# Kernel tuning notes

Hardware: AMD Instinct MI355X
Metric: run time of the kernel (lower is better)

Reference implementation:

```python
import jax, jax.numpy as jnp
import numpy as np

B, L, W = 64, 20, 48
D = W * W           # 2304, MoE input/output size (image_width**2)
E = 4               # num_experts
HID = 2 * D         # expert hidden size
K = 1               # top_k
LOSS_COEF = 1e-2


def _cv_squared(x):
    # torch: x.var() (unbiased) / (x.mean()**2 + eps)
    eps = 1e-10
    return jnp.var(x, ddof=1) / (jnp.mean(x) ** 2 + eps)


def _moe(x, w_gate, w1, b1, w2, b2):
    # Noisy top-k gating, inference path (train=False => clean logits, no noise).
    logits = x @ w_gate                                   # [B, E]
    top_logits, top_idx = jax.lax.top_k(logits, K + 1)    # min(k+1, E)
    topk_gates = jax.nn.softmax(top_logits[:, :K], axis=-1)
    gates = jnp.zeros_like(logits).at[
        jnp.arange(x.shape[0])[:, None], top_idx[:, :K]
    ].set(topk_gates)                                     # [B, E] sparse gates
    importance = gates.sum(0)
    load = (gates > 0).sum(0).astype(x.dtype)             # _gates_to_load
    aux = LOSS_COEF * (_cv_squared(importance) + _cv_squared(load))
    # Dense expert compute weighted by gates (same math as dispatch/combine).
    h = jax.nn.relu(jnp.einsum('bd,edh->beh', x, w1) + b1)      # [B,E,HID]
    y = jnp.einsum('beh,ehd->bed', h, w2) + b2                  # [B,E,D]
    out = jnp.einsum('be,bed->bd', gates, y)                    # [B,D]
    return out, aux


def _conv3d(x, w, b, pad):
    y = jax.lax.conv_general_dilated(
        x, w, window_strides=(1, 1, 1), padding=pad,
        dimension_numbers=('NCDHW', 'OIDHW', 'NCDHW'))
    return y + b[None, :, None, None, None]


def _forward(input, conv1_w, conv1_b, conv2_w, conv2_b,
             t_gate, t_w1, t_b1, t_w2, t_b2,
             a_gate, a_w1, a_b1, a_w2, a_b2,
             q_gate, q_w1, q_b1, q_w2, q_b2,
             enc_w, enc_b, dec_w, dec_b):
    x = jnp.transpose(input, (0, 2, 1, 3, 4))                   # [B,1,L,H,W]
    x = jax.nn.relu(_conv3d(x, conv1_w, conv1_b, ((1, 1), (1, 1), (1, 1))))
    x = jax.nn.relu(_conv3d(x, conv2_w, conv2_b, ((0, 0), (1, 1), (1, 1))))  # [B,1,1,H,W]
    xf = x.reshape(x.shape[0], -1)                              # [B, D]
    transform, l1 = _moe(xf, t_gate, t_w1, t_b1, t_w2, t_b2)
    add, l2 = _moe(xf, a_gate, a_w1, a_b1, a_w2, a_b2)
    quad, l3 = _moe(xf, q_gate, q_w1, q_b1, q_w2, q_b2)
    s = input.shape                                             # [B,L,1,H,W]
    transform = transform.reshape(s[0], 1, s[2], s[3], s[4])
    add = add.reshape(s[0], 1, s[2], s[3], s[4])
    quad = quad.reshape(s[0], 1, s[2], s[3], s[4])
    out = input * input * quad + input * transform + add        # [B,L,1,H,W]
    # encoder = Linear(D,D)+ReLU, decoder = Linear(D,D) over flattened H*W
    of = out.reshape(s[0], s[1], D)
    of = jax.nn.relu(of @ enc_w + enc_b)
    of = of @ dec_w + dec_b
    of = jax.nn.sigmoid(of)
    return of.reshape(s), l1 + l2 + l3


def setup_inputs() -> dict:
    key = jax.random.key(0)
    ks = jax.random.split(key, 32)
    sc = 0.02
    inp = {
        'input': jax.random.normal(ks[0], (B, L, 1, W, W), jnp.float32),
        'conv1_w': jax.random.normal(ks[1], (10, 1, 3, 3, 3), jnp.float32) * sc,
        'conv1_b': jnp.zeros((10,), jnp.float32),
        'conv2_w': jax.random.normal(ks[2], (1, 10, L, 3, 3), jnp.float32) * sc,
        'conv2_b': jnp.zeros((1,), jnp.float32),
        'enc_w': jax.random.normal(ks[3], (D, D), jnp.float32) * sc,
        'enc_b': jnp.zeros((D,), jnp.float32),
        'dec_w': jax.random.normal(ks[4], (D, D), jnp.float32) * sc,
        'dec_b': jnp.zeros((D,), jnp.float32),
    }
    for i, p in enumerate(['t', 'a', 'q']):
        k0, k1, k2 = jax.random.split(ks[5 + i], 3)
        inp[p + '_gate'] = jnp.zeros((D, E), jnp.float32) + jax.random.normal(k0, (D, E), jnp.float32) * sc
        inp[p + '_w1'] = jax.random.normal(k1, (E, D, HID), jnp.float32) * sc
        inp[p + '_b1'] = jnp.zeros((E, HID), jnp.float32)
        inp[p + '_w2'] = jax.random.normal(k2, (E, HID, D), jnp.float32) * sc
        inp[p + '_b2'] = jnp.zeros((E, D), jnp.float32)
    return inp


def reference(input, conv1_w, conv1_b, conv2_w, conv2_b,
              t_gate, t_w1, t_b1, t_w2, t_b2,
              a_gate, a_w1, a_b1, a_w2, a_b2,
              q_gate, q_w1, q_b1, q_w2, q_b2,
              enc_w, enc_b, dec_w, dec_b):
    return _forward(input, conv1_w, conv1_b, conv2_w, conv2_b,
                    t_gate, t_w1, t_b1, t_w2, t_b2,
                    a_gate, a_w1, a_b1, a_w2, a_b2,
                    q_gate, q_w1, q_b1, q_w2, q_b2,
                    enc_w, enc_b, dec_w, dec_b)
```

## Files before the change

kernel.cpp:

```cpp
#include <hip/hip_runtime.h>
#include <stdint.h>

#define NB 64
#define NL 20
#define ND 2304
#define NE 4
#define NH 4608
#define NM 1280

typedef float f32x4 __attribute__((ext_vector_type(4)));
typedef __bf16 bf16x8 __attribute__((ext_vector_type(8)));
typedef unsigned short u16;
typedef u16 u16x4 __attribute__((ext_vector_type(4)));
typedef unsigned int u32;
typedef u32 u32x4 __attribute__((ext_vector_type(4)));

__device__ __forceinline__ u16 f2bf(float f) {
  u32 u = __builtin_bit_cast(u32, f);
  u += 0x7fffu + ((u >> 16) & 1u);
  return (u16)(u >> 16);
}

#define OFF_XFACC 0
#define OFF_XF    147456
#define OFF_H     294912
#define OFF_Y     1179648
#define OFF_AUX   1622016
#define OFF_CNT   1622020
#define OFF_ROWS  1622032
#define OFF_OFB   1622240
#define OFF_H1B   3096800
#define OFF_ENCWB 4571360
#define OFF_DECWB 7225568
#define OFF_XC    9879776
#define OFF_P     10322144

__global__ __launch_bounds__(256) void k_zero(float* __restrict__ p) {
  p[(size_t)blockIdx.x * 256 + threadIdx.x] = 0.f;
}

__global__ __launch_bounds__(256) void k_conv(
    const float* __restrict__ in, const float* __restrict__ w1,
    const float* __restrict__ b1, const float* __restrict__ w2,
    float* __restrict__ xf_acc) {
  __shared__ float insl[3][50][50];
  __shared__ float c1[2][50][50];
  __shared__ float w1s[270];
  __shared__ float w2s[90];
  __shared__ float b1s[10];
  const int d = blockIdx.x, b = blockIdx.y, t = threadIdx.x;
  for (int i = t; i < 270; i += 256) w1s[i] = w1[i];
  for (int i = t; i < 90; i += 256) w2s[i] = w2[(size_t)((i / 9) * 20 + d) * 9 + (i % 9)];
  if (t < 10) b1s[t] = b1[t];
  for (int i = t; i < 7500; i += 256) {
    int s = i / 2500, rr = (i % 2500) / 50, cc = i % 50;
    int gd = d - 1 + s, gy = rr - 1, gx = cc - 1;
    float v = 0.f;
    if (gd >= 0 && gd < NL && (unsigned)gy < 48u && (unsigned)gx < 48u)
      v = in[((size_t)b * NL + gd) * ND + gy * 48 + gx];
    insl[s][rr][cc] = v;
  }
  for (int i = t; i < 5000; i += 256) ((float*)c1)[i] = 0.f;
  float s2[3][4];
#pragma unroll
  for (int qi = 0; qi < 3; ++qi)
#pragma unroll
    for (int xq = 0; xq < 4; ++xq) s2[qi][xq] = 0.f;
  __syncthreads();
  for (int pc = 0; pc < 5; ++pc) {
#pragma unroll
    for (int qi = 0; qi < 3; ++qi) {
      int q = t + qi * 256;
      if (q < 576) {
        int y = q / 12, x0 = (q % 12) * 4;
        float a0[4], a1[4];
        const float bb0 = b1s[2 * pc], bb1 = b1s[2 * pc + 1];
#pragma unroll
        for (int xq = 0; xq < 4; ++xq) { a0[xq] = bb0; a1[xq] = bb1; }
#pragma unroll
        for (int kd = 0; kd < 3; ++kd)
#pragma unroll
          for (int ky = 0; ky < 3; ++ky) {
            float v[6];
#pragma unroll
            for (int i = 0; i < 6; ++i) v[i] = insl[kd][y + ky][x0 + i];
            const float* wa = &w1s[(2 * pc) * 27 + kd * 9 + ky * 3];
            const float* wb = wa + 27;
#pragma unroll
            for (int xq = 0; xq < 4; ++xq) {
              a0[xq] += v[xq] * wa[0] + v[xq + 1] * wa[1] + v[xq + 2] * wa[2];
              a1[xq] += v[xq] * wb[0] + v[xq + 1] * wb[1] + v[xq + 2] * wb[2];
            }
          }
#pragma unroll
        for (int xq = 0; xq < 4; ++xq) {
          c1[0][y + 1][x0 + 1 + xq] = fmaxf(a0[xq], 0.f);
          c1[1][y + 1][x0 + 1 + xq] = fmaxf(a1[xq], 0.f);
        }
      }
    }
    __syncthreads();
#pragma unroll
    for (int qi = 0; qi < 3; ++qi) {
      int q = t + qi * 256;
      if (q < 576) {
        int y = q / 12, x0 = (q % 12) * 4;
#pragma unroll
        for (int cc = 0; cc < 2; ++cc) {
#pragma unroll
          for (int ky = 0; ky < 3; ++ky) {
            float v[6];
#pragma unroll
            for (int i = 0; i < 6; ++i) v[i] = c1[cc][y + ky][x0 + i];
            const float* wr = &w2s[(2 * pc + cc) * 9 + ky * 3];
#pragma unroll
            for (int xq = 0; xq < 4; ++xq)
              s2[qi][xq] += v[xq] * wr[0] + v[xq + 1] * wr[1] + v[xq + 2] * wr[2];
          }
        }
      }
    }
    __syncthreads();
  }
#pragma unroll
  for (int qi = 0; qi < 3; ++qi) {
    int q = t + qi * 256;
    if (q < 576) {
#pragma unroll
      for (int xq = 0; xq < 4; ++xq)
        atomicAdd(&xf_acc[(size_t)b * ND + q * 4 + xq], s2[qi][xq]);
    }
  }
}

__global__ __launch_bounds__(256) void k_bias_relu(
    const float* __restrict__ acc, const float* __restrict__ c2b, float* __restrict__ xf) {
  size_t i = (size_t)blockIdx.x * 256 + threadIdx.x;
  xf[i] = fmaxf(acc[i] + c2b[0], 0.f);
}

__global__ __launch_bounds__(256) void k_gate(
    const float* __restrict__ xf,
    const float* __restrict__ g0, const float* __restrict__ g1, const float* __restrict__ g2,
    float* __restrict__ aux, int* __restrict__ cnt, int* __restrict__ rows) {
  const int p = blockIdx.x, t = threadIdx.x;
  const float* __restrict__ g = (p == 0) ? g0 : ((p == 1) ? g1 : g2);
  __shared__ float lg[64][4];
  __shared__ int lidx[64];
  __shared__ int lcnt[4];
  if (t < 4) lcnt[t] = 0;
  const int wv = t >> 6, l = t & 63;
  for (int b0 = 0; b0 < 64; b0 += 4) {
    int bb = b0 + wv;
    f32x4 acc = {0.f, 0.f, 0.f, 0.f};
    const float* xr = xf + (size_t)bb * ND + l * 36;
    const float* gr = g + (size_t)l * 36 * 4;
#pragma unroll
    for (int i4 = 0; i4 < 9; ++i4) {
      f32x4 xv = *(const f32x4*)(xr + i4 * 4);
#pragma unroll
      for (int qq = 0; qq < 4; ++qq) {
        f32x4 gv = *(const f32x4*)(gr + (i4 * 4 + qq) * 4);
        acc += xv[qq] * gv;
      }
    }
#pragma unroll
    for (int e = 0; e < 4; ++e) {
      float pv = acc[e];
#pragma unroll
      for (int off = 32; off > 0; off >>= 1) pv += __shfl_down(pv, off);
      if (l == 0) lg[bb][e] = pv;
    }
  }
  __syncthreads();
  if (t < 64) {
    float best = lg[t][0];
    int bi = 0;
#pragma unroll
    for (int e = 1; e < 4; ++e)
      if (lg[t][e] > best) { best = lg[t][e]; bi = e; }
    lidx[t] = bi;
    atomicAdd(&lcnt[bi], 1);
  }
  __syncthreads();
  if (t == 0) {
    int ofs[4]; int run = 0;
#pragma unroll
    for (int e = 0; e < 4; ++e) { ofs[e] = run; run += lcnt[e]; cnt[p * 4 + e] = lcnt[e]; }
    for (int b = 0; b < 64; ++b) { int e = lidx[b]; rows[p * 64 + ofs[e]++] = b; }
    float var = 0.f;
#pragma unroll
    for (int e = 0; e < 4; ++e) { float dd = (float)lcnt[e] - 16.f; var += dd * dd; }
    var *= (1.f / 3.f);
    aux[p] = 0.02f * var / (256.f + 1e-10f);
  }
}

__global__ __launch_bounds__(256) void k_gather(
    const float* __restrict__ xf, const int* __restrict__ rows, float* __restrict__ Xc) {
  const int slot = blockIdx.x, t = threadIdx.x;
  const int p = slot >> 6;
  const int r = rows[slot];
  const f32x4* src = (const f32x4*)(xf + ((size_t)(p * 0 + r)) * ND);
  f32x4* dst = (f32x4*)(Xc + (size_t)slot * ND);
  for (int i = t; i < ND / 4; i += 256) dst[i] = src[i];
}

template <int K, int N, int KS>
__global__ __launch_bounds__(256) void k_moe_stream(
    const float* __restrict__ Xc,
    const float* __restrict__ wt, const float* __restrict__ wa, const float* __restrict__ wq,
    const int* __restrict__ cnt, float* __restrict__ P) {
  constexpr int KL = K / KS;
  constexpr int KW = KL / 4;
  const int tile = blockIdx.x;
  const int ks = blockIdx.y;
  const int pe = blockIdx.z >> 1, ch = blockIdx.z & 1;
  const int p = pe >> 2, e = pe & 3;
  const int c = cnt[p * 4 + e];
  const int rstart = ch * 32;
  if (rstart >= c) return;
  const int nrows = min(32, c - rstart);
  int pref = 0;
  for (int e2 = 0; e2 < e; ++e2) pref += cnt[p * 4 + e2];
  const int slot0 = p * 64 + pref + rstart;
  const float* __restrict__ W = (p == 0) ? wt : ((p == 1) ? wa : wq);
  __shared__ float xs[32][KL + 4];
  const int t = threadIdx.x;
  for (int i = t; i < 32 * (KL / 4); i += 256) {
    int r = i / (KL / 4), kq = (i - r * (KL / 4)) * 4;
    int slot = slot0 + r; if (slot > 191) slot = 191;
    *(f32x4*)(&xs[r][kq]) = *(const f32x4*)(Xc + (size_t)slot * K + ks * KL + kq);
  }
  __syncthreads();
  const int w = t >> 6, l = t & 63;
  const int j0 = tile * 128 + l * 2;
  const float* __restrict__ wp = W + (size_t)e * K * N + (size_t)(ks * KL + w * KW) * N + j0;
  const int kloc = w * KW;
  float acc0[32], acc1[32];
#pragma unroll
  for (int r = 0; r < 32; ++r) { acc0[r] = 0.f; acc1[r] = 0.f; }
  for (int kb = 0; kb < KW; kb += 4) {
    float2 wv0 = *(const float2*)(wp + (size_t)(kb + 0) * N);
    float2 wv1 = *(const float2*)(wp + (size_t)(kb + 1) * N);
    float2 wv2 = *(const float2*)(wp + (size_t)(kb + 2) * N);
    float2 wv3 = *(const float2*)(wp + (size_t)(kb + 3) * N);
#pragma unroll
    for (int rg = 0; rg < 8; ++rg) {
      if (rg * 4 < nrows) {
#pragma unroll
        for (int rr = 0; rr < 4; ++rr) {
          const int r = rg * 4 + rr;
          f32x4 xv = *(const f32x4*)(&xs[r][kloc + kb]);
          acc0[r] = fmaf(xv[0], wv0.x, acc0[r]);
          acc1[r] = fmaf(xv[0], wv0.y, acc1[r]);
          acc0[r] = fmaf(xv[1], wv1.x, acc0[r]);
          acc1[r] = fmaf(xv[1], wv1.y, acc1[r]);
          acc0[r] = fmaf(xv[2], wv2.x, acc0[r]);
          acc1[r] = fmaf(xv[2], wv2.y, acc1[r]);
          acc0[r] = fmaf(xv[3], wv3.x, acc0[r]);
          acc1[r] = fmaf(xv[3], wv3.y, acc1[r]);
        }
      }
    }
  }
  float* red = &xs[0][0];
  const size_t pbase = (size_t)ks * 192 * N;
#pragma unroll
  for (int b = 0; b < 4; ++b) {
    __syncthreads();
#pragma unroll
    for (int rr = 0; rr < 8; ++rr) {
      const int r = b * 8 + rr;
      *(float2*)(&red[((w * 8 + rr) * 64 + l) * 2]) = make_float2(acc0[r], acc1[r]);
    }
    __syncthreads();
#pragma unroll
    for (int s = 0; s < 2; ++s) {
      const int rr = w * 2 + s;
      const int r = b * 8 + rr;
      if (r < nrows) {
        float2 s0 = *(const float2*)(&red[((0 * 8 + rr) * 64 + l) * 2]);
        float2 s1 = *(const float2*)(&red[((1 * 8 + rr) * 64 + l) * 2]);
        float2 s2 = *(const float2*)(&red[((2 * 8 + rr) * 64 + l) * 2]);
        float2 s3 = *(const float2*)(&red[((3 * 8 + rr) * 64 + l) * 2]);
        float2 o = make_float2(s0.x + s1.x + s2.x + s3.x, s0.y + s1.y + s2.y + s3.y);
        *(float2*)(P + pbase + (size_t)(slot0 + r) * N + j0) = o;
      }
    }
  }
}

__global__ __launch_bounds__(256) void k_red1(
    const float* __restrict__ P,
    const float* __restrict__ b1t, const float* __restrict__ b1a, const float* __restrict__ b1q,
    const int* __restrict__ cnt, float* __restrict__ H) {
  const int slot = blockIdx.y;
  const int p = slot >> 6, pos = slot & 63;
  int e = 0, run = cnt[p * 4];
  while (pos >= run && e < 3) { ++e; run += cnt[p * 4 + e]; }
  const float* __restrict__ b1 = (p == 0) ? b1t : ((p == 1) ? b1a : b1q);
  const int j0 = blockIdx.x * 1024 + threadIdx.x * 4;
  if (j0 >= NH) return;
  f32x4 s = *(const f32x4*)(b1 + (size_t)e * NH + j0);
#pragma unroll
  for (int ks = 0; ks < 8; ++ks)
    s += *(const f32x4*)(P + ((size_t)ks * 192 + slot) * NH + j0);
  f32x4 r;
#pragma unroll
  for (int q = 0; q < 4; ++q) r[q] = fmaxf(s[q], 0.f);
  *(f32x4*)(H + (size_t)slot * NH + j0) = r;
}

__global__ __launch_bounds__(256) void k_red2(
    const float* __restrict__ P,
    const float* __restrict__ b2t, const float* __restrict__ b2a, const float* __restrict__ b2q,
    const int* __restrict__ cnt, const int* __restrict__ rows, float* __restrict__ Y) {
  const int slot = blockIdx.y;
  const int p = slot >> 6, pos = slot & 63;
  int e = 0, run = cnt[p * 4];
  while (pos >= run && e < 3) { ++e; run += cnt[p * 4 + e]; }
  const float* __restrict__ b2 = (p == 0) ? b2t : ((p == 1) ? b2a : b2q);
  const int b = rows[slot];
  const int t = threadIdx.x;
  if (t >= 192) return;
  const int j0 = blockIdx.x * 768 + t * 4;
  f32x4 s = *(const f32x4*)(b2 + (size_t)e * ND + j0);
#pragma unroll
  for (int ks = 0; ks < 16; ++ks)
    s += *(const f32x4*)(P + ((size_t)ks * 192 + slot) * ND + j0);
  *(f32x4*)(Y + (size_t)(p * 64 + b) * ND + j0) = s;
}

__global__ __launch_bounds__(256) void k_combine(
    const float* __restrict__ in, const float* __restrict__ Y, u16* __restrict__ ofb) {
  const size_t i = (size_t)blockIdx.x * 256 + threadIdx.x;
  const size_t e0 = i * 4;
  const int row = (int)(e0 / ND);
  const int d = (int)(e0 - (size_t)row * ND);
  const int b = row / NL;
  f32x4 v = *(const f32x4*)(in + e0);
  const size_t yb = (size_t)b * ND + d;
  f32x4 tt = *(const f32x4*)(Y + yb);
  f32x4 aa = *(const f32x4*)(Y + (size_t)64 * ND + yb);
  f32x4 qq = *(const f32x4*)(Y + (size_t)128 * ND + yb);
  u16x4 o;
#pragma unroll
  for (int q = 0; q < 4; ++q) {
    float f = v[q] * v[q] * qq[q] + v[q] * tt[q] + aa[q];
    o[q] = f2bf(f);
  }
  *(u16x4*)(ofb + e0) = o;
}

__global__ __launch_bounds__(256) void k_wt(
    const float* __restrict__ encw, const float* __restrict__ decw,
    u16* __restrict__ encb, u16* __restrict__ decb) {
  __shared__ float tl[32][33];
  const float* __restrict__ src = blockIdx.z ? decw : encw;
  u16* __restrict__ dst = blockIdx.z ? decb : encb;
  const int k0 = blockIdx.x * 32, n0 = blockIdx.y * 32;
  const int tx = threadIdx.x & 31, ty = threadIdx.x >> 5;
  for (int r = ty; r < 32; r += 8) tl[r][tx] = src[(size_t)(k0 + r) * ND + n0 + tx];
  __syncthreads();
  for (int r = ty; r < 32; r += 8) dst[(size_t)(n0 + r) * ND + k0 + tx] = f2bf(tl[tx][r]);
}

template <int MODE>
__global__ __launch_bounds__(256) void k_gemm(
    const u16* __restrict__ A, const u16* __restrict__ Bt,
    const float* __restrict__ bias, void* __restrict__ outp,
    const float* __restrict__ aux) {
  __shared__ u16 As[128 * 32];
  __shared__ u16 Bs[128 * 32];
  const int t = threadIdx.x;
  const int bm = blockIdx.x, bn = blockIdx.y;
  const int lane = t & 63;
  const int wr = (t >> 7) & 1, wc = (t >> 6) & 1;
  const int l15 = lane & 15, l4 = lane >> 4;
  f32x4 acc[4][4] = {};
  const int r0 = t >> 2, kc0 = (t & 3) * 8;
  const int r1 = (t + 256) >> 2, kc1 = ((t + 256) & 3) * 8;
  const size_t baseA = (size_t)(bm * 128) * ND;
  const size_t baseB = (size_t)(bn * 128) * ND;
  for (int k0 = 0; k0 < ND; k0 += 32) {
    *(u32x4*)(As + t * 8) = *(const u32x4*)(A + baseA + (size_t)r0 * ND + k0 + kc0);
    *(u32x4*)(Bs + t * 8) = *(const u32x4*)(Bt + baseB + (size_t)r0 * ND + k0 + kc0);
    *(u32x4*)(As + (t + 256) * 8) = *(const u32x4*)(A + baseA + (size_t)r1 * ND + k0 + kc1);
    *(u32x4*)(Bs + (t + 256) * 8) = *(const u32x4*)(Bt + baseB + (size_t)r1 * ND + k0 + kc1);
    __syncthreads();
    bf16x8 af[4], bfr[4];
#pragma unroll
    for (int i = 0; i < 4; ++i) {
      af[i] = *(const bf16x8*)(As + (wr * 64 + i * 16 + l15) * 32 + l4 * 8);
      bfr[i] = *(const bf16x8*)(Bs + (wc * 64 + i * 16 + l15) * 32 + l4 * 8);
    }
#pragma unroll
    for (int mi = 0; mi < 4; ++mi)
#pragma unroll
      for (int ni = 0; ni < 4; ++ni)
        acc[mi][ni] = __builtin_amdgcn_mfma_f32_16x16x32_bf16(af[mi], bfr[ni], acc[mi][ni], 0, 0, 0);
    __syncthreads();
  }
  const int colbase = bn * 128 + wc * 64;
  const int rowbase = bm * 128 + wr * 64;
#pragma unroll
  for (int mi = 0; mi < 4; ++mi) {
#pragma unroll
    for (int ni = 0; ni < 4; ++ni) {
      const int colg = colbase + ni * 16 + l15;
      const float bv = bias[colg];
#pragma unroll
      for (int r = 0; r < 4; ++r) {
        const int rowg = rowbase + mi * 16 + l4 * 4 + r;
        float v = acc[mi][ni][r] + bv;
        if (MODE == 0) {
          ((u16*)outp)[(size_t)rowg * ND + colg] = f2bf(fmaxf(v, 0.f));
        } else {
          ((float*)outp)[(size_t)rowg * ND + colg] = 1.f / (1.f + __expf(-v));
        }
      }
    }
  }
  if (MODE == 1 && bm == 0 && bn == 0 && t == 0)
    ((float*)outp)[(size_t)NM * ND] = aux[0] + aux[1] + aux[2];
}

extern "C" void kernel_launch(void* const* d_in, const int* in_sizes, int n_in,
                              void* d_out, int out_size, void* d_ws, size_t ws_size,
                              hipStream_t stream) {
  (void)in_sizes; (void)n_in; (void)out_size; (void)ws_size;
  const float* input   = (const float*)d_in[0];
  const float* conv1_w = (const float*)d_in[1];
  const float* conv1_b = (const float*)d_in[2];
  const float* conv2_w = (const float*)d_in[3];
  const float* conv2_b = (const float*)d_in[4];
  const float* enc_w   = (const float*)d_in[5];
  const float* enc_b   = (const float*)d_in[6];
  const float* dec_w   = (const float*)d_in[7];
  const float* dec_b   = (const float*)d_in[8];
  const float* gate_t = (const float*)d_in[9];
  const float* w1_t   = (const float*)d_in[10];
  const float* b1_t   = (const float*)d_in[11];
  const float* w2_t   = (const float*)d_in[12];
  const float* b2_t   = (const float*)d_in[13];
  const float* gate_a = (const float*)d_in[14];
  const float* w1_a   = (const float*)d_in[15];
  const float* b1_a   = (const float*)d_in[16];
  const float* w2_a   = (const float*)d_in[17];
  const float* b2_a   = (const float*)d_in[18];
  const float* gate_q = (const float*)d_in[19];
  const float* w1_q   = (const float*)d_in[20];
  const float* b1_q   = (const float*)d_in[21];
  const float* w2_q   = (const float*)d_in[22];
  const float* b2_q   = (const float*)d_in[23];

  float* ws = (float*)d_ws;
  float* xf_acc = ws + OFF_XFACC;
  float* xf     = ws + OFF_XF;
  float* H      = ws + OFF_H;
  float* Y      = ws + OFF_Y;
  float* aux    = ws + OFF_AUX;
  int*   cnt    = (int*)(ws + OFF_CNT);
  int*   rows   = (int*)(ws + OFF_ROWS);
  u16*   ofb    = (u16*)(ws + OFF_OFB);
  u16*   h1b    = (u16*)(ws + OFF_H1B);
  u16*   encwb  = (u16*)(ws + OFF_ENCWB);
  u16*   decwb  = (u16*)(ws + OFF_DECWB);
  float* Xc     = ws + OFF_XC;
  float* P      = ws + OFF_P;

  k_zero<<<576, 256, 0, stream>>>(xf_acc);
  k_conv<<<dim3(20, 64), 256, 0, stream>>>(input, conv1_w, conv1_b, conv2_w, xf_acc);
  k_bias_relu<<<576, 256, 0, stream>>>(xf_acc, conv2_b, xf);
  k_wt<<<dim3(72, 72, 2), 256, 0, stream>>>(enc_w, dec_w, encwb, decwb);
  k_gate<<<3, 256, 0, stream>>>(xf, gate_t, gate_a, gate_q, aux, cnt, rows);
  k_gather<<<192, 256, 0, stream>>>(xf, rows, Xc);
  k_moe_stream<ND, NH, 8><<<dim3(36, 8, 24), 256, 0, stream>>>(Xc, w1_t, w1_a, w1_q, cnt, P);
  k_red1<<<dim3(5, 192), 256, 0, stream>>>(P, b1_t, b1_a, b1_q, cnt, H);
  k_moe_stream<NH, ND, 16><<<dim3(18, 16, 24), 256, 0, stream>>>(H, w2_t, w2_a, w2_q, cnt, P);
  k_red2<<<dim3(3, 192), 256, 0, stream>>>(P, b2_t, b2_a, b2_q, cnt, rows, Y);
  k_combine<<<2880, 256, 0, stream>>>(input, Y, ofb);
  k_gemm<0><<<dim3(10, 18), 256, 0, stream>>>(ofb, encwb, enc_b, (void*)h1b, aux);
  k_gemm<1><<<dim3(10, 18), 256, 0, stream>>>(h1b, decwb, dec_b, d_out, aux);
}
```

Baseline: 573.6 us.

## Double-buffer MoE expert GEMM tiles via direct global-to-LDS loads

Restructures the streaming MoE GEMM kernel so that X and weight tiles of 32 k-values are loaded into double-buffered shared memory with global_load_lds, and the next tile's load overlaps compute on the current one. Each wave now owns 8 rows across the full k-range instead of all 32 rows over a quarter of k, which removes the cross-wave shared-memory reduction and its many barriers. The intent is to hide weight-streaming latency and cut register pressure from 64 accumulators down to 16. The trade-off is a barrier per k-tile, and the early skip of empty row groups is gone, so padded rows are computed anyway.

```diff
diff --git a/kernel.cpp b/kernel.cpp
--- a/kernel.cpp
+++ b/kernel.cpp
@@ -19,6 +19,12 @@
   u32 u = __builtin_bit_cast(u32, f);
   u += 0x7fffu + ((u >> 16) & 1u);
   return (u16)(u >> 16);
+}
+
+__device__ __forceinline__ void gl_lds16(const void* g, void* l) {
+  __builtin_amdgcn_global_load_lds(
+      (const __attribute__((address_space(1))) void*)g,
+      (__attribute__((address_space(3))) void*)l, 16, 0, 0);
 }
 
 #define OFF_XFACC 0
@@ -199,9 +205,8 @@
 __global__ __launch_bounds__(256) void k_gather(
     const float* __restrict__ xf, const int* __restrict__ rows, float* __restrict__ Xc) {
   const int slot = blockIdx.x, t = threadIdx.x;
-  const int p = slot >> 6;
   const int r = rows[slot];
-  const f32x4* src = (const f32x4*)(xf + ((size_t)(p * 0 + r)) * ND);
+  const f32x4* src = (const f32x4*)(xf + (size_t)r * ND);
   f32x4* dst = (f32x4*)(Xc + (size_t)slot * ND);
   for (int i = t; i < ND / 4; i += 256) dst[i] = src[i];
 }
@@ -212,7 +217,7 @@
     const float* __restrict__ wt, const float* __restrict__ wa, const float* __restrict__ wq,
     const int* __restrict__ cnt, float* __restrict__ P) {
   constexpr int KL = K / KS;
-  constexpr int KW = KL / 4;
+  constexpr int NT = KL / 32;
   const int tile = blockIdx.x;
   const int ks = blockIdx.y;
   const int pe = blockIdx.z >> 1, ch = blockIdx.z & 1;
@@ -225,69 +230,69 @@
   for (int e2 = 0; e2 < e; ++e2) pref += cnt[p * 4 + e2];
   const int slot0 = p * 64 + pref + rstart;
   const float* __restrict__ W = (p == 0) ? wt : ((p == 1) ? wa : wq);
-  __shared__ float xs[32][KL + 4];
+  __shared__ float xsb[2][32 * 32];
+  __shared__ float wtb[2][32 * 128];
   const int t = threadIdx.x;
-  for (int i = t; i < 32 * (KL / 4); i += 256) {
-    int r = i / (KL / 4), kq = (i - r * (KL / 4)) * 4;
-    int slot = slot0 + r; if (slot > 191) slot = 191;
-    *(f32x4*)(&xs[r][kq]) = *(const f32x4*)(Xc + (size_t)slot * K + ks * KL + kq);
-  }
+  const int w = t >> 6, l = t & 63;
+  int slotc = slot0 + (t >> 3); if (slotc > 191) slotc = 191;
+  const float* Xg = Xc + (size_t)slotc * K + ks * KL + (t & 7) * 4;
+  const float* Wg = W + (size_t)e * K * N + (size_t)(ks * KL + (t >> 5)) * N
+                      + tile * 128 + (t & 31) * 4;
+
+#define STAGE(BUF, KT)                                                        \
+  {                                                                           \
+    const int k0_ = (KT) * 32;                                                \
+    gl_lds16(Xg + k0_, &xsb[BUF][t * 4]);                                     \
+    _Pragma("unroll")                                                         \
+    for (int q = 0; q < 4; ++q)                                               \
+      gl_lds16(Wg + (size_t)(k0_ + q * 8) * N, &wtb[BUF][q * 1024 + t * 4]);  \
+  }
+
+  float2 acc[8];
+#pragma unroll
+  for (int r = 0; r < 8; ++r) acc[r] = make_float2(0.f, 0.f);
+  const int wrow = w * 8;
+  const int colp = l * 2;
+
+  STAGE(0, 0);
+  asm volatile("s_waitcnt vmcnt(0)" ::: "memory");
   __syncthreads();
-  const int w = t >> 6, l = t & 63;
-  const int j0 = tile * 128 + l * 2;
-  const float* __restrict__ wp = W + (size_t)e * K * N + (size_t)(ks * KL + w * KW) * N + j0;
-  const int kloc = w * KW;
-  float acc0[32], acc1[32];
-#pragma unroll
-  for (int r = 0; r < 32; ++r) { acc0[r] = 0.f; acc1[r] = 0.f; }
-  for (int kb = 0; kb < KW; kb += 4) {
-    float2 wv0 = *(const float2*)(wp + (size_t)(kb + 0) * N);
-    float2 wv1 = *(const float2*)(wp + (size_t)(kb + 1) * N);
-    float2 wv2 = *(const float2*)(wp + (size_t)(kb + 2) * N);
-    float2 wv3 = *(const float2*)(wp + (size_t)(kb + 3) * N);
-#pragma unroll
-    for (int rg = 0; rg < 8; ++rg) {
-      if (rg * 4 < nrows) {
-#pragma unroll
-        for (int rr = 0; rr < 4; ++rr) {
-          const int r = rg * 4 + rr;
-          f32x4 xv = *(const f32x4*)(&xs[r][kloc + kb]);
-          acc0[r] = fmaf(xv[0], wv0.x, acc0[r]);
-          acc1[r] = fmaf(xv[0], wv0.y, acc1[r]);
-          acc0[r] = fmaf(xv[1], wv1.x, acc0[r]);
-          acc1[r] = fmaf(xv[1], wv1.y, acc1[r]);
-          acc0[r] = fmaf(xv[2], wv2.x, acc0[r]);
-          acc1[r] = fmaf(xv[2], wv2.y, acc1[r]);
-          acc0[r] = fmaf(xv[3], wv3.x, acc0[r]);
-          acc1[r] = fmaf(xv[3], wv3.y, acc1[r]);
-        }
+
+#pragma unroll 1
+  for (int kt = 0; kt < NT; ++kt) {
+    const int cur = kt & 1;
+    if (kt + 1 < NT) STAGE(cur ^ 1, kt + 1);
+    const float* xw = &xsb[cur][0];
+    const float* ww = &wtb[cur][0];
+#pragma unroll
+    for (int k4 = 0; k4 < 8; ++k4) {
+      float2 w0 = *(const float2*)(ww + (k4 * 4 + 0) * 128 + colp);
+      float2 w1 = *(const float2*)(ww + (k4 * 4 + 1) * 128 + colp);
+      float2 w2v = *(const float2*)(ww + (k4 * 4 + 2) * 128 + colp);
+      float2 w3v = *(const float2*)(ww + (k4 * 4 + 3) * 128 + colp);
+#pragma unroll
+      for (int r = 0; r < 8; ++r) {
+        f32x4 xv = *(const f32x4*)(xw + (wrow + r) * 32 + k4 * 4);
+        acc[r].x = fmaf(xv[0], w0.x, acc[r].x);
+        acc[r].y = fmaf(xv[0], w0.y, acc[r].y);
+        acc[r].x = fmaf(xv[1], w1.x, acc[r].x);
+        acc[r].y = fmaf(xv[1], w1.y, acc[r].y);
+        acc[r].x = fmaf(xv[2], w2v.x, acc[r].x);
+        acc[r].y = fmaf(xv[2], w2v.y, acc[r].y);
+        acc[r].x = fmaf(xv[3], w3v.x, acc[r].x);
+        acc[r].y = fmaf(xv[3], w3v.y, acc[r].y);
       }
     }
-  }
-  float* red = &xs[0][0];
+    asm volatile("s_waitcnt vmcnt(0)" ::: "memory");
+    __syncthreads();
+  }
+#undef STAGE
+
   const size_t pbase = (size_t)ks * 192 * N;
 #pragma unroll
-  for (int b = 0; b < 4; ++b) {
-    __syncthreads();
-#pragma unroll
-    for (int rr = 0; rr < 8; ++rr) {
-      const int r = b * 8 + rr;
-      *(float2*)(&red[((w * 8 + rr) * 64 + l) * 2]) = make_float2(acc0[r], acc1[r]);
-    }
-    __syncthreads();
-#pragma unroll
-    for (int s = 0; s < 2; ++s) {
-      const int rr = w * 2 + s;
-      const int r = b * 8 + rr;
-      if (r < nrows) {
-        float2 s0 = *(const float2*)(&red[((0 * 8 + rr) * 64 + l) * 2]);
-        float2 s1 = *(const float2*)(&red[((1 * 8 + rr) * 64 + l) * 2]);
-        float2 s2 = *(const float2*)(&red[((2 * 8 + rr) * 64 + l) * 2]);
-        float2 s3 = *(const float2*)(&red[((3 * 8 + rr) * 64 + l) * 2]);
-        float2 o = make_float2(s0.x + s1.x + s2.x + s3.x, s0.y + s1.y + s2.y + s3.y);
-        *(float2*)(P + pbase + (size_t)(slot0 + r) * N + j0) = o;
-      }
-    }
+  for (int r = 0; r < 8; ++r) {
+    if (wrow + r < nrows)
+      *(float2*)(P + pbase + (size_t)(slot0 + wrow + r) * N + tile * 128 + colp) = acc[r];
   }
 }
 
```

Result: slower. 595.8 us (+3.9%).
